# Optimization experiments

Measured on AMD Instinct MI355X. Metric: run time of the kernel, lower is better.

## Reference

```python
import jax, jax.numpy as jnp
import numpy as np

DIM_Q, DIM_K, HEADS = 256, 32, 4
SCALE = (DIM_Q // HEADS) ** (-0.5)


def setup_inputs() -> dict:
    key = jax.random.key(0)
    ks = jax.random.split(key, 12)
    B, C, H, W, D = 2, DIM_Q, 16, 16, 16
    inp = {
        'F_VNet': jax.random.normal(ks[0], (B, C, H, W, D), dtype=jnp.float32),
        'F_Knowledge': jax.random.normal(ks[1], (B, DIM_K, H, W, D), dtype=jnp.float32),
        # torch nn.Linear: y = x @ W.T + b, W: [out, in]
        'Wq': jax.random.normal(ks[2], (DIM_Q, DIM_Q), dtype=jnp.float32) * (DIM_Q ** -0.5),
        'bq': jnp.zeros((DIM_Q,), dtype=jnp.float32),
        'Wk': jax.random.normal(ks[3], (DIM_Q, DIM_K), dtype=jnp.float32) * (DIM_K ** -0.5),
        'bk': jnp.zeros((DIM_Q,), dtype=jnp.float32),
        'Wv': jax.random.normal(ks[4], (DIM_Q, DIM_K), dtype=jnp.float32) * (DIM_K ** -0.5),
        'bv': jnp.zeros((DIM_Q,), dtype=jnp.float32),
        'Wo': jax.random.normal(ks[5], (DIM_Q, DIM_Q), dtype=jnp.float32) * (DIM_Q ** -0.5),
        'bo': jnp.zeros((DIM_Q,), dtype=jnp.float32),
    }
    return inp


def reference(F_VNet, F_Knowledge, Wq, bq, Wk, bk, Wv, bv, Wo, bo):
    B, C, H, W, D = F_VNet.shape
    Ck = F_Knowledge.shape[1]
    # flatten spatial dims to tokens: [B, N, C]
    xq = F_VNet.reshape(B, C, -1).transpose(0, 2, 1)          # [B, Nq, dim_q]
    xk = F_Knowledge.reshape(B, Ck, -1).transpose(0, 2, 1)    # [B, Nk, dim_k]
    Q = xq @ Wq.T + bq                                        # [B, Nq, dim_q]
    K = xk @ Wk.T + bk                                        # [B, Nk, dim_q]
    V = xk @ Wv.T + bv                                        # [B, Nk, dim_q]
    attn = jax.nn.softmax(jnp.einsum('bqc,bkc->bqk', Q, K) * SCALE, axis=-1)
    out = jnp.einsum('bqk,bkc->bqc', attn, V)                 # [B, Nq, dim_q]
    out = out @ Wo.T + bo
    out = out.transpose(0, 2, 1).reshape(B, C, H, W, D)
    return F_VNet + out
```

## Files before the change

kernel.cpp:

```cpp
#include <hip/hip_runtime.h>
#include <hip/hip_bf16.h>
#include <cstdint>
#include <cstddef>

#define N_TOK 4096
#define CQ    256
#define CK    32

typedef __attribute__((ext_vector_type(4))) float  f32x4;
typedef __attribute__((ext_vector_type(8))) __bf16 bf16x8;
typedef __attribute__((ext_vector_type(4))) short  s16x4;

__device__ __forceinline__ unsigned short f2bf(float f) {
  union { float f; unsigned u; } x; x.f = f;
  unsigned r = x.u + 0x7FFFu + ((x.u >> 16) & 1u);
  return (unsigned short)(r >> 16);
}

__device__ __forceinline__ f32x4 mfma16(bf16x8 a, bf16x8 b, f32x4 c) {
  return __builtin_amdgcn_mfma_f32_16x16x32_bf16(a, b, c, 0, 0, 0);
}

__device__ __forceinline__ int pos2key(int pos) {
  return ((pos >> 3) << 2) + (pos & 3) + (((pos >> 2) & 1) << 4);
}

__global__ __launch_bounds__(256) void prep_kernel(
    const float* __restrict__ Wq, const float* __restrict__ bq,
    const float* __restrict__ Wk, const float* __restrict__ Wv,
    const float* __restrict__ bv, const float* __restrict__ Wo,
    const float* __restrict__ bo, const float* __restrict__ Fk,
    unsigned short* __restrict__ Aqkt, float* __restrict__ bqk,
    unsigned short* __restrict__ W2bf, float* __restrict__ c2,
    unsigned short* __restrict__ Vpv, unsigned short* __restrict__ XkT)
{
  __shared__ float red[256];
  __shared__ unsigned short trs[128][33];
  const int blk = blockIdx.x, t = threadIdx.x;
  if (blk < 32) {
    const int j = blk;
    float acc = 0.f;
    #pragma unroll 8
    for (int i = 0; i < CQ; i++)
      acc = fmaf(Wq[(size_t)i * CQ + t], Wk[(size_t)i * CK + j], acc);
    Aqkt[(size_t)j * CQ + t] = f2bf(0.125f * acc);
    red[t] = bq[t] * Wk[(size_t)t * CK + j];
    __syncthreads();
    for (int s = 128; s > 0; s >>= 1) {
      if (t < s) red[t] += red[t + s];
      __syncthreads();
    }
    if (t == 0) bqk[j] = 0.125f * red[0];
  } else if (blk < 64) {
    const int j = blk - 32;
    float acc = 0.f, acc2 = 0.f;
    #pragma unroll 8
    for (int i = 0; i < CQ; i++) {
      float wo = Wo[(size_t)t * CQ + i];
      acc  = fmaf(wo, Wv[(size_t)i * CK + j], acc);
      acc2 = fmaf(wo, bv[i], acc2);
    }
    W2bf[(size_t)t * CK + j] = f2bf(acc);
    if (j == 0) c2[t] = bo[t] + acc2;
  } else {
    const int blk2 = blk - 64;
    const int b = blk2 >> 5;
    const int t0 = (blk2 & 31) << 7;
    #pragma unroll
    for (int i = 0; i < 4; i++) {
      int flat = (i * 256 + t) << 2;
      int r = flat >> 7, c4 = flat & 127;
      float4 v = *(const float4*)(Fk + ((size_t)(b * CK + r)) * N_TOK + t0 + c4);
      ushort4 u = { f2bf(v.x), f2bf(v.y), f2bf(v.z), f2bf(v.w) };
      trs[c4][r] = u.x; trs[c4+1][r] = u.y; trs[c4+2][r] = u.z; trs[c4+3][r] = u.w;
    }
    __syncthreads();
    {
      const int token = t >> 1, half = t & 1;
      unsigned short tmp[16] __attribute__((aligned(16)));
      #pragma unroll
      for (int k = 0; k < 16; k++) tmp[k] = trs[token][half * 16 + k];
      unsigned short* dst = XkT + ((size_t)(b * N_TOK + t0 + token)) * CK + half * 16;
      ((uint4*)dst)[0] = ((const uint4*)tmp)[0];
      ((uint4*)dst)[1] = ((const uint4*)tmp)[1];
    }
    {
      const int ch32l = t >> 6, d = (t & 63) >> 1, ph = t & 1;
      unsigned short tmp[16] __attribute__((aligned(16)));
      #pragma unroll
      for (int i = 0; i < 16; i++) {
        int pos = ph * 16 + i;
        tmp[i] = trs[ch32l * 32 + pos2key(pos)][d];
      }
      unsigned short* dst = Vpv +
          (((size_t)(b * 128 + (t0 >> 5) + ch32l)) * 32 + d) * 32 + ph * 16;
      ((uint4*)dst)[0] = ((const uint4*)tmp)[0];
      ((uint4*)dst)[1] = ((const uint4*)tmp)[1];
    }
  }
}

__global__ __launch_bounds__(128) void qproj_kernel(
    const float* __restrict__ X, const unsigned short* __restrict__ Aqkt,
    const float* __restrict__ bqk, unsigned short* __restrict__ QN)
{
  __shared__ unsigned short bs[32][40];
  const int b = blockIdx.x >> 7;
  const int t0 = (blockIdx.x & 127) << 5;
  const int t = threadIdx.x, w = t >> 6;
  const int lane = t & 63, c = lane & 15, g = lane >> 4;
  f32x4 acc[2] = {};
  for (int k0 = 0; k0 < CQ; k0 += 32) {
    #pragma unroll
    for (int i = 0; i < 2; i++) {
      int flat = (i * 128 + t) << 2;
      int cc = flat >> 5, tk = flat & 31;
      float4 v = *(const float4*)(X + ((size_t)(b * CQ + k0 + cc)) * N_TOK + t0 + tk);
      bs[tk  ][cc] = f2bf(v.x); bs[tk+1][cc] = f2bf(v.y);
      bs[tk+2][cc] = f2bf(v.z); bs[tk+3][cc] = f2bf(v.w);
    }
    __syncthreads();
    bf16x8 a = *(const bf16x8*)&bs[w * 16 + c][g * 8];
    #pragma unroll
    for (int nt = 0; nt < 2; nt++) {
      bf16x8 bB = *(const bf16x8*)(Aqkt + (size_t)(nt * 16 + c) * CQ + k0 + g * 8);
      acc[nt] = mfma16(a, bB, acc[nt]);
    }
    __syncthreads();
  }
  #pragma unroll
  for (int nt = 0; nt < 2; nt++) {
    float bj = bqk[nt * 16 + c];
    #pragma unroll
    for (int r = 0; r < 4; r++)
      QN[((size_t)(b * N_TOK + t0 + w * 16 + g * 4 + r)) * CK + nt * 16 + c] =
          f2bf(acc[nt][r] + bj);
  }
}

__global__ __launch_bounds__(256, 4) void flash_kernel(
    const unsigned short* __restrict__ QN, const unsigned short* __restrict__ XkT,
    const unsigned short* __restrict__ Vpv, float* __restrict__ partO,
    float* __restrict__ partML)
{
  __shared__ unsigned short ks[512 * 40] __attribute__((aligned(16)));
  const int blk = blockIdx.x;
  const int b   = blk >> 9;
  const int qg  = (blk >> 3) & 63;
  const int ksp = blk & 7;
  const int t = threadIdx.x, w = t >> 6;
  const int lane = t & 63, c = lane & 15, g = lane >> 4;
  const int t0 = qg * 64 + w * 16;
  const int gk0 = ksp * 512;

  {
    const unsigned short* src = XkT + ((size_t)(b * N_TOK + gk0)) * CK;
    #pragma unroll
    for (int r = 0; r < 8; r++) {
      int flat = r * 256 + t;
      int row = flat >> 2, part = flat & 3;
      *(uint4*)(ks + row * 40 + part * 8) = *(const uint4*)(src + (size_t)flat * 8);
    }
  }
  const bf16x8 qf = *(const bf16x8*)(QN + ((size_t)(b * N_TOK + t0 + c)) * CK + g * 8);
  __syncthreads();

  const unsigned short* vp = Vpv + (size_t)b * 128 * 1024;
  float mO = -1e30f, lO = 0.f;
  f32x4 O0 = {}, O1 = {};

  #pragma unroll
  for (int pass = 0; pass < 2; pass++) {
    const int pk = pass * 256;

    f32x4 s[4][4];
    #pragma unroll
    for (int it = 0; it < 4; it++)
      #pragma unroll
      for (int nt = 0; nt < 4; nt++) {
        bf16x8 ak = *(const bf16x8*)&ks[(pk + it * 64 + nt * 16 + c) * 40 + g * 8];
        f32x4 z = {};
        s[it][nt] = mfma16(ak, qf, z);
      }

    float mx = -1e30f;
    #pragma unroll
    for (int it = 0; it < 4; it++)
      #pragma unroll
      for (int nt = 0; nt < 4; nt++)
        mx = fmaxf(mx, fmaxf(fmaxf(s[it][nt][0], s[it][nt][1]),
                             fmaxf(s[it][nt][2], s[it][nt][3])));
    mx = fmaxf(mx, __shfl_xor(mx, 16));
    mx = fmaxf(mx, __shfl_xor(mx, 32));

    float l = 0.f;
    s16x4 pf[4][4];
    #pragma unroll
    for (int it = 0; it < 4; it++)
      #pragma unroll
      for (int nt = 0; nt < 4; nt++) {
        float p0 = __expf(s[it][nt][0] - mx);
        float p1 = __expf(s[it][nt][1] - mx);
        float p2 = __expf(s[it][nt][2] - mx);
        float p3 = __expf(s[it][nt][3] - mx);
        l += (p0 + p1) + (p2 + p3);
        union { __hip_bfloat162 h2[2]; s16x4 v; } pu;
        pu.h2[0] = __float22bfloat162_rn(make_float2(p0, p1));
        pu.h2[1] = __float22bfloat162_rn(make_float2(p2, p3));
        pf[it][nt] = pu.v;
      }
    l += __shfl_xor(l, 16);
    l += __shfl_xor(l, 32);

    f32x4 o0 = {}, o1 = {};
    #pragma unroll
    for (int it = 0; it < 4; it++)
      #pragma unroll
      for (int ntp = 0; ntp < 2; ntp++) {
        const int ch32 = (gk0 + pk + it * 64 + ntp * 32) >> 5;
        const unsigned short* base = vp + (size_t)ch32 * 1024;
        union { s16x4 h[2]; bf16x8 v; } bu;
        bu.h[0] = pf[it][ntp * 2];
        bu.h[1] = pf[it][ntp * 2 + 1];
        bf16x8 a0 = *(const bf16x8*)(base + c * 32 + g * 8);
        bf16x8 a1 = *(const bf16x8*)(base + (16 + c) * 32 + g * 8);
        o0 = mfma16(a0, bu.v, o0);
        o1 = mfma16(a1, bu.v, o1);
      }

    float mN = fmaxf(mO, mx);
    float fO = __expf(mO - mN), fP = __expf(mx - mN);
    lO = lO * fO + l * fP;
    #pragma unroll
    for (int r = 0; r < 4; r++) {
      O0[r] = O0[r] * fO + o0[r] * fP;
      O1[r] = O1[r] * fO + o1[r] * fP;
    }
    mO = mN;
  }

  float* po = partO + (size_t)blk * 2048 + (w * 16 + c) * 32;
  *(f32x4*)(po + g * 4)      = O0;
  *(f32x4*)(po + 16 + g * 4) = O1;
  if (lane < 16) {
    partML[(size_t)blk * 128 + w * 16 + lane]      = mO;
    partML[(size_t)blk * 128 + 64 + w * 16 + lane] = lO;
  }
}

__global__ __launch_bounds__(256) void oproj_kernel(
    const float* __restrict__ partO, const float* __restrict__ partML,
    const unsigned short* __restrict__ W2bf, const float* __restrict__ c2,
    const float* __restrict__ X, float* __restrict__ Y)
{
  __shared__ unsigned short ons[32][40];
  const int blk = blockIdx.x;
  const int b = blk >> 7, tt = blk & 127;
  const int t = threadIdx.x, w = t >> 6;
  const int lane = t & 63, c = lane & 15, g = lane >> 4;
  const int t0 = tt * 32;

  {
    const int tl32 = t >> 3, ch4 = t & 7;
    const int q  = t0 + tl32;
    const int qg = q >> 6, tl = q & 63;
    const int blkbase = (b << 9) + qg * 8;
    float mv[8], lv[8], mM = -1e30f;
    #pragma unroll
    for (int k = 0; k < 8; k++) {
      mv[k] = partML[(size_t)(blkbase + k) * 128 + tl];
      lv[k] = partML[(size_t)(blkbase + k) * 128 + 64 + tl];
      mM = fmaxf(mM, mv[k]);
    }
    float lsum = 0.f, f[8];
    #pragma unroll
    for (int k = 0; k < 8; k++) {
      f[k] = __expf(mv[k] - mM);
      lsum = fmaf(f[k], lv[k], lsum);
    }
    const float inv = 1.0f / lsum;
    float acc[4] = {};
    #pragma unroll
    for (int k = 0; k < 8; k++) {
      float4 v = *(const float4*)(partO + (size_t)(blkbase + k) * 2048 + tl * 32 + ch4 * 4);
      acc[0] = fmaf(f[k], v.x, acc[0]); acc[1] = fmaf(f[k], v.y, acc[1]);
      acc[2] = fmaf(f[k], v.z, acc[2]); acc[3] = fmaf(f[k], v.w, acc[3]);
    }
    ons[tl32][ch4 * 4    ] = f2bf(acc[0] * inv);
    ons[tl32][ch4 * 4 + 1] = f2bf(acc[1] * inv);
    ons[tl32][ch4 * 4 + 2] = f2bf(acc[2] * inv);
    ons[tl32][ch4 * 4 + 3] = f2bf(acc[3] * inv);
  }
  __syncthreads();

  const int m0 = w * 64;
  bf16x8 bB[2];
  #pragma unroll
  for (int nt = 0; nt < 2; nt++)
    bB[nt] = *(const bf16x8*)&ons[nt * 16 + c][g * 8];
  f32x4 acc[4][2] = {};
  #pragma unroll
  for (int mt = 0; mt < 4; mt++) {
    bf16x8 aW = *(const bf16x8*)(W2bf + (size_t)(m0 + mt * 16 + c) * CK + g * 8);
    acc[mt][0] = mfma16(aW, bB[0], acc[mt][0]);
    acc[mt][1] = mfma16(aW, bB[1], acc[mt][1]);
  }
  #pragma unroll
  for (int mt = 0; mt < 4; mt++)
    #pragma unroll
    for (int r = 0; r < 4; r++) {
      const int row = m0 + mt * 16 + g * 4 + r;
      const float cc = c2[row];
      #pragma unroll
      for (int nt = 0; nt < 2; nt++) {
        size_t idx = ((size_t)(b * CQ + row)) * N_TOK + t0 + nt * 16 + c;
        Y[idx] = acc[mt][nt][r] + cc + X[idx];
      }
    }
}

extern "C" void kernel_launch(void* const* d_in, const int* in_sizes, int n_in,
                              void* d_out, int out_size, void* d_ws, size_t ws_size,
                              hipStream_t stream) {
  const float* F  = (const float*)d_in[0];
  const float* Fk = (const float*)d_in[1];
  const float* Wq = (const float*)d_in[2];
  const float* bq = (const float*)d_in[3];
  const float* Wk = (const float*)d_in[4];
  const float* Wv = (const float*)d_in[6];
  const float* bv = (const float*)d_in[7];
  const float* Wo = (const float*)d_in[8];
  const float* bo = (const float*)d_in[9];
  float* Y = (float*)d_out;
  char* ws = (char*)d_ws;
  unsigned short* XkT   = (unsigned short*)(ws);
  unsigned short* Vpv   = (unsigned short*)(ws + (512u << 10));
  unsigned short* QN    = (unsigned short*)(ws + (1536u << 10));
  unsigned short* Aqkt  = (unsigned short*)(ws + (2048u << 10));
  unsigned short* W2bf  = (unsigned short*)(ws + (2080u << 10));
  float*          bqk   = (float*)(ws + (2112u << 10));
  float*          c2    = (float*)(ws + (2116u << 10));
  float*          partO = (float*)(ws + (4096u << 10));
  float*          partML= (float*)(ws + (16384u << 10));

  prep_kernel <<<128,  256, 0, stream>>>(Wq, bq, Wk, Wv, bv, Wo, bo, Fk,
                                         Aqkt, bqk, W2bf, c2, Vpv, XkT);
  qproj_kernel<<<256,  128, 0, stream>>>(F, Aqkt, bqk, QN);
  flash_kernel<<<1024, 256, 0, stream>>>(QN, XkT, Vpv, partO, partML);
  oproj_kernel<<<256,  256, 0, stream>>>(partO, partML, W2bf, c2, F, Y);
}
```

Baseline: 129.4 us.

## Fuse Q projection, flash attention and output projection into one kernel

Merges the qproj, flash-attention and oproj kernels into a single fused kernel. Each 32-query block computes Q in LDS, streams all 4096 keys in 8 chunks with register double-buffering, splits the key range across two wave pairs, merges their partial softmax states in LDS, then applies the output projection and residual. This removes the partO/partML round trips, the QN buffer and two launches. The trade-off is a grid of only 256 blocks at one block per CU, which lowers parallelism compared with the 1024-block split-K flash kernel. The softmax scale now folds log2(e) so exp2 can be used, and two prep unroll factors change.

```diff
diff --git a/kernel.cpp b/kernel.cpp
--- a/kernel.cpp
+++ b/kernel.cpp
@@ -6,6 +6,7 @@
 #define N_TOK 4096
 #define CQ    256
 #define CK    32
+#define QK_SCALE 0.18033688011112042f
 
 typedef __attribute__((ext_vector_type(4))) float  f32x4;
 typedef __attribute__((ext_vector_type(8))) __bf16 bf16x8;
@@ -19,6 +20,19 @@
 
 __device__ __forceinline__ f32x4 mfma16(bf16x8 a, bf16x8 b, f32x4 c) {
   return __builtin_amdgcn_mfma_f32_16x16x32_bf16(a, b, c, 0, 0, 0);
+}
+
+__device__ __forceinline__ float exp2fast(float x) {
+#if __has_builtin(__builtin_amdgcn_exp2f)
+  return __builtin_amdgcn_exp2f(x);
+#else
+  float r; asm("v_exp_f32 %0, %1" : "=v"(r) : "v"(x)); return r;
+#endif
+}
+
+__device__ __forceinline__ void bar_lds() {
+  asm volatile("s_waitcnt lgkmcnt(0)" ::: "memory");
+  __builtin_amdgcn_s_barrier();
 }
 
 __device__ __forceinline__ int pos2key(int pos) {
@@ -40,21 +54,21 @@
   if (blk < 32) {
     const int j = blk;
     float acc = 0.f;
-    #pragma unroll 8
+    #pragma unroll 16
     for (int i = 0; i < CQ; i++)
       acc = fmaf(Wq[(size_t)i * CQ + t], Wk[(size_t)i * CK + j], acc);
-    Aqkt[(size_t)j * CQ + t] = f2bf(0.125f * acc);
+    Aqkt[(size_t)j * CQ + t] = f2bf(QK_SCALE * acc);
     red[t] = bq[t] * Wk[(size_t)t * CK + j];
     __syncthreads();
     for (int s = 128; s > 0; s >>= 1) {
       if (t < s) red[t] += red[t + s];
       __syncthreads();
     }
-    if (t == 0) bqk[j] = 0.125f * red[0];
+    if (t == 0) bqk[j] = QK_SCALE * red[0];
   } else if (blk < 64) {
     const int j = blk - 32;
     float acc = 0.f, acc2 = 0.f;
-    #pragma unroll 8
+    #pragma unroll 16
     for (int i = 0; i < CQ; i++) {
       float wo = Wo[(size_t)t * CQ + i];
       acc  = fmaf(wo, Wv[(size_t)i * CK + j], acc);
@@ -100,87 +114,95 @@
   }
 }
 
-__global__ __launch_bounds__(128) void qproj_kernel(
+__global__ __launch_bounds__(256, 1) void fused_kernel(
     const float* __restrict__ X, const unsigned short* __restrict__ Aqkt,
-    const float* __restrict__ bqk, unsigned short* __restrict__ QN)
+    const float* __restrict__ bqk, const unsigned short* __restrict__ XkT,
+    const unsigned short* __restrict__ Vpv,
+    const unsigned short* __restrict__ W2bf, const float* __restrict__ c2,
+    float* __restrict__ Y)
 {
-  __shared__ unsigned short bs[32][40];
-  const int b = blockIdx.x >> 7;
+  __shared__ union {
+    unsigned short ks[512 * 40];
+    unsigned short bs8[8][32][40];
+  } u __attribute__((aligned(16)));
+  __shared__ unsigned short qn[32][40] __attribute__((aligned(16)));
+  __shared__ float mlx[2][2][16];
+  __shared__ float ofx[2][16][32];
+
+  const int b  = blockIdx.x >> 7;
   const int t0 = (blockIdx.x & 127) << 5;
   const int t = threadIdx.x, w = t >> 6;
   const int lane = t & 63, c = lane & 15, g = lane >> 4;
-  f32x4 acc[2] = {};
-  for (int k0 = 0; k0 < CQ; k0 += 32) {
-    #pragma unroll
-    for (int i = 0; i < 2; i++) {
-      int flat = (i * 128 + t) << 2;
-      int cc = flat >> 5, tk = flat & 31;
-      float4 v = *(const float4*)(X + ((size_t)(b * CQ + k0 + cc)) * N_TOK + t0 + tk);
-      bs[tk  ][cc] = f2bf(v.x); bs[tk+1][cc] = f2bf(v.y);
-      bs[tk+2][cc] = f2bf(v.z); bs[tk+3][cc] = f2bf(v.w);
-    }
-    __syncthreads();
-    bf16x8 a = *(const bf16x8*)&bs[w * 16 + c][g * 8];
+  const int tw = w & 1, kh = w >> 1;
+  const int pk = kh << 8;
+
+  #pragma unroll
+  for (int i = 0; i < 8; i++) {
+    int flat = i * 256 + t;
+    int cc = flat >> 3, tk = (flat & 7) << 2;
+    float4 v = *(const float4*)(X + ((size_t)(b * CQ + cc)) * N_TOK + t0 + tk);
+    int kk = cc >> 5, chl = cc & 31;
+    u.bs8[kk][tk    ][chl] = f2bf(v.x);
+    u.bs8[kk][tk + 1][chl] = f2bf(v.y);
+    u.bs8[kk][tk + 2][chl] = f2bf(v.z);
+    u.bs8[kk][tk + 3][chl] = f2bf(v.w);
+  }
+  const unsigned short* xksrc = XkT + ((size_t)b * N_TOK) * CK;
+  uint4 R[8];
+  #pragma unroll
+  for (int r = 0; r < 8; r++)
+    R[r] = *(const uint4*)(xksrc + (size_t)(r * 256 + t) * 8);
+  bar_lds();
+
+  if (w < 2) {
+    f32x4 qacc[2] = {};
+    #pragma unroll
+    for (int kk = 0; kk < 8; kk++) {
+      bf16x8 a = *(const bf16x8*)&u.bs8[kk][w * 16 + c][g * 8];
+      #pragma unroll
+      for (int nt = 0; nt < 2; nt++) {
+        bf16x8 bB = *(const bf16x8*)(Aqkt + (size_t)(nt * 16 + c) * CQ + kk * 32 + g * 8);
+        qacc[nt] = mfma16(a, bB, qacc[nt]);
+      }
+    }
     #pragma unroll
     for (int nt = 0; nt < 2; nt++) {
-      bf16x8 bB = *(const bf16x8*)(Aqkt + (size_t)(nt * 16 + c) * CQ + k0 + g * 8);
-      acc[nt] = mfma16(a, bB, acc[nt]);
-    }
-    __syncthreads();
-  }
-  #pragma unroll
-  for (int nt = 0; nt < 2; nt++) {
-    float bj = bqk[nt * 16 + c];
-    #pragma unroll
-    for (int r = 0; r < 4; r++)
-      QN[((size_t)(b * N_TOK + t0 + w * 16 + g * 4 + r)) * CK + nt * 16 + c] =
-          f2bf(acc[nt][r] + bj);
-  }
-}
-
-__global__ __launch_bounds__(256, 4) void flash_kernel(
-    const unsigned short* __restrict__ QN, const unsigned short* __restrict__ XkT,
-    const unsigned short* __restrict__ Vpv, float* __restrict__ partO,
-    float* __restrict__ partML)
-{
-  __shared__ unsigned short ks[512 * 40] __attribute__((aligned(16)));
-  const int blk = blockIdx.x;
-  const int b   = blk >> 9;
-  const int qg  = (blk >> 3) & 63;
-  const int ksp = blk & 7;
-  const int t = threadIdx.x, w = t >> 6;
-  const int lane = t & 63, c = lane & 15, g = lane >> 4;
-  const int t0 = qg * 64 + w * 16;
-  const int gk0 = ksp * 512;
-
-  {
-    const unsigned short* src = XkT + ((size_t)(b * N_TOK + gk0)) * CK;
+      float bj = bqk[nt * 16 + c];
+      #pragma unroll
+      for (int r = 0; r < 4; r++)
+        qn[w * 16 + g * 4 + r][nt * 16 + c] = f2bf(qacc[nt][r] + bj);
+    }
+  }
+  bar_lds();
+
+  const bf16x8 qf = *(const bf16x8*)&qn[tw * 16 + c][g * 8];
+  const unsigned short* vp = Vpv + (size_t)b * 128 * 1024;
+
+  float mO = -1e30f, lO = 0.f;
+  f32x4 O0 = {}, O1 = {};
+
+  for (int s = 0; s < 8; s++) {
     #pragma unroll
     for (int r = 0; r < 8; r++) {
       int flat = r * 256 + t;
-      int row = flat >> 2, part = flat & 3;
-      *(uint4*)(ks + row * 40 + part * 8) = *(const uint4*)(src + (size_t)flat * 8);
-    }
-  }
-  const bf16x8 qf = *(const bf16x8*)(QN + ((size_t)(b * N_TOK + t0 + c)) * CK + g * 8);
-  __syncthreads();
-
-  const unsigned short* vp = Vpv + (size_t)b * 128 * 1024;
-  float mO = -1e30f, lO = 0.f;
-  f32x4 O0 = {}, O1 = {};
-
-  #pragma unroll
-  for (int pass = 0; pass < 2; pass++) {
-    const int pk = pass * 256;
-
-    f32x4 s[4][4];
+      *(uint4*)(u.ks + (flat >> 2) * 40 + (flat & 3) * 8) = R[r];
+    }
+    if (s < 7) {
+      const unsigned short* nsrc = xksrc + (size_t)(s + 1) * (512 * CK);
+      #pragma unroll
+      for (int r = 0; r < 8; r++)
+        R[r] = *(const uint4*)(nsrc + (size_t)(r * 256 + t) * 8);
+    }
+    bar_lds();
+
+    f32x4 sc[4][4];
     #pragma unroll
     for (int it = 0; it < 4; it++)
       #pragma unroll
       for (int nt = 0; nt < 4; nt++) {
-        bf16x8 ak = *(const bf16x8*)&ks[(pk + it * 64 + nt * 16 + c) * 40 + g * 8];
+        bf16x8 ak = *(const bf16x8*)&u.ks[(pk + it * 64 + nt * 16 + c) * 40 + g * 8];
         f32x4 z = {};
-        s[it][nt] = mfma16(ak, qf, z);
+        sc[it][nt] = mfma16(ak, qf, z);
       }
 
     float mx = -1e30f;
@@ -188,8 +210,8 @@
     for (int it = 0; it < 4; it++)
       #pragma unroll
       for (int nt = 0; nt < 4; nt++)
-        mx = fmaxf(mx, fmaxf(fmaxf(s[it][nt][0], s[it][nt][1]),
-                             fmaxf(s[it][nt][2], s[it][nt][3])));
+        mx = fmaxf(mx, fmaxf(fmaxf(sc[it][nt][0], sc[it][nt][1]),
+                             fmaxf(sc[it][nt][2], sc[it][nt][3])));
     mx = fmaxf(mx, __shfl_xor(mx, 16));
     mx = fmaxf(mx, __shfl_xor(mx, 32));
 
@@ -199,10 +221,10 @@
     for (int it = 0; it < 4; it++)
       #pragma unroll
       for (int nt = 0; nt < 4; nt++) {
-        float p0 = __expf(s[it][nt][0] - mx);
-        float p1 = __expf(s[it][nt][1] - mx);
-        float p2 = __expf(s[it][nt][2] - mx);
-        float p3 = __expf(s[it][nt][3] - mx);
+        float p0 = exp2fast(sc[it][nt][0] - mx);
+        float p1 = exp2fast(sc[it][nt][1] - mx);
+        float p2 = exp2fast(sc[it][nt][2] - mx);
+        float p3 = exp2fast(sc[it][nt][3] - mx);
         l += (p0 + p1) + (p2 + p3);
         union { __hip_bfloat162 h2[2]; s16x4 v; } pu;
         pu.h2[0] = __float22bfloat162_rn(make_float2(p0, p1));
@@ -217,7 +239,7 @@
     for (int it = 0; it < 4; it++)
       #pragma unroll
       for (int ntp = 0; ntp < 2; ntp++) {
-        const int ch32 = (gk0 + pk + it * 64 + ntp * 32) >> 5;
+        const int ch32 = (s << 4) + (kh << 3) + it * 2 + ntp;
         const unsigned short* base = vp + (size_t)ch32 * 1024;
         union { s16x4 h[2]; bf16x8 v; } bu;
         bu.h[0] = pf[it][ntp * 2];
@@ -229,7 +251,7 @@
       }
 
     float mN = fmaxf(mO, mx);
-    float fO = __expf(mO - mN), fP = __expf(mx - mN);
+    float fO = exp2fast(mO - mN), fP = exp2fast(mx - mN);
     lO = lO * fO + l * fP;
     #pragma unroll
     for (int r = 0; r < 4; r++) {
@@ -237,84 +259,54 @@
       O1[r] = O1[r] * fO + o1[r] * fP;
     }
     mO = mN;
-  }
-
-  float* po = partO + (size_t)blk * 2048 + (w * 16 + c) * 32;
-  *(f32x4*)(po + g * 4)      = O0;
-  *(f32x4*)(po + 16 + g * 4) = O1;
-  if (lane < 16) {
-    partML[(size_t)blk * 128 + w * 16 + lane]      = mO;
-    partML[(size_t)blk * 128 + 64 + w * 16 + lane] = lO;
-  }
-}
-
-__global__ __launch_bounds__(256) void oproj_kernel(
-    const float* __restrict__ partO, const float* __restrict__ partML,
-    const unsigned short* __restrict__ W2bf, const float* __restrict__ c2,
-    const float* __restrict__ X, float* __restrict__ Y)
-{
-  __shared__ unsigned short ons[32][40];
-  const int blk = blockIdx.x;
-  const int b = blk >> 7, tt = blk & 127;
-  const int t = threadIdx.x, w = t >> 6;
-  const int lane = t & 63, c = lane & 15, g = lane >> 4;
-  const int t0 = tt * 32;
-
-  {
-    const int tl32 = t >> 3, ch4 = t & 7;
-    const int q  = t0 + tl32;
-    const int qg = q >> 6, tl = q & 63;
-    const int blkbase = (b << 9) + qg * 8;
-    float mv[8], lv[8], mM = -1e30f;
-    #pragma unroll
-    for (int k = 0; k < 8; k++) {
-      mv[k] = partML[(size_t)(blkbase + k) * 128 + tl];
-      lv[k] = partML[(size_t)(blkbase + k) * 128 + 64 + tl];
-      mM = fmaxf(mM, mv[k]);
-    }
-    float lsum = 0.f, f[8];
-    #pragma unroll
-    for (int k = 0; k < 8; k++) {
-      f[k] = __expf(mv[k] - mM);
-      lsum = fmaf(f[k], lv[k], lsum);
-    }
-    const float inv = 1.0f / lsum;
-    float acc[4] = {};
-    #pragma unroll
-    for (int k = 0; k < 8; k++) {
-      float4 v = *(const float4*)(partO + (size_t)(blkbase + k) * 2048 + tl * 32 + ch4 * 4);
-      acc[0] = fmaf(f[k], v.x, acc[0]); acc[1] = fmaf(f[k], v.y, acc[1]);
-      acc[2] = fmaf(f[k], v.z, acc[2]); acc[3] = fmaf(f[k], v.w, acc[3]);
-    }
-    ons[tl32][ch4 * 4    ] = f2bf(acc[0] * inv);
-    ons[tl32][ch4 * 4 + 1] = f2bf(acc[1] * inv);
-    ons[tl32][ch4 * 4 + 2] = f2bf(acc[2] * inv);
-    ons[tl32][ch4 * 4 + 3] = f2bf(acc[3] * inv);
+    bar_lds();
+  }
+
+  if (kh == 1) {
+    if (lane < 16) { mlx[tw][0][c] = mO; mlx[tw][1][c] = lO; }
+    #pragma unroll
+    for (int r = 0; r < 4; r++) {
+      ofx[tw][c][g * 4 + r]      = O0[r];
+      ofx[tw][c][16 + g * 4 + r] = O1[r];
+    }
   }
   __syncthreads();
+  if (kh == 0) {
+    float m1 = mlx[tw][0][c], l1 = mlx[tw][1][c];
+    float mN = fmaxf(mO, m1);
+    float f0 = exp2fast(mO - mN), f1 = exp2fast(m1 - mN);
+    float inv = 1.0f / (lO * f0 + l1 * f1);
+    f0 *= inv; f1 *= inv;
+    #pragma unroll
+    for (int r = 0; r < 4; r++) {
+      qn[tw * 16 + c][g * 4 + r]      = f2bf(O0[r] * f0 + ofx[tw][c][g * 4 + r] * f1);
+      qn[tw * 16 + c][16 + g * 4 + r] = f2bf(O1[r] * f0 + ofx[tw][c][16 + g * 4 + r] * f1);
+    }
+  }
+  __syncthreads();
 
   const int m0 = w * 64;
-  bf16x8 bB[2];
+  bf16x8 wb[2];
   #pragma unroll
   for (int nt = 0; nt < 2; nt++)
-    bB[nt] = *(const bf16x8*)&ons[nt * 16 + c][g * 8];
-  f32x4 acc[4][2] = {};
+    wb[nt] = *(const bf16x8*)&qn[nt * 16 + c][g * 8];
+  f32x4 acc2[4][2] = {};
   #pragma unroll
   for (int mt = 0; mt < 4; mt++) {
     bf16x8 aW = *(const bf16x8*)(W2bf + (size_t)(m0 + mt * 16 + c) * CK + g * 8);
-    acc[mt][0] = mfma16(aW, bB[0], acc[mt][0]);
-    acc[mt][1] = mfma16(aW, bB[1], acc[mt][1]);
+    acc2[mt][0] = mfma16(aW, wb[0], acc2[mt][0]);
+    acc2[mt][1] = mfma16(aW, wb[1], acc2[mt][1]);
   }
   #pragma unroll
   for (int mt = 0; mt < 4; mt++)
     #pragma unroll
     for (int r = 0; r < 4; r++) {
       const int row = m0 + mt * 16 + g * 4 + r;
-      const float cc = c2[row];
+      const float cc2 = c2[row];
       #pragma unroll
       for (int nt = 0; nt < 2; nt++) {
         size_t idx = ((size_t)(b * CQ + row)) * N_TOK + t0 + nt * 16 + c;
-        Y[idx] = acc[mt][nt][r] + cc + X[idx];
+        Y[idx] = acc2[mt][nt][r] + cc2 + X[idx];
       }
     }
 }
@@ -335,17 +327,12 @@
   char* ws = (char*)d_ws;
   unsigned short* XkT   = (unsigned short*)(ws);
   unsigned short* Vpv   = (unsigned short*)(ws + (512u << 10));
-  unsigned short* QN    = (unsigned short*)(ws + (1536u << 10));
   unsigned short* Aqkt  = (unsigned short*)(ws + (2048u << 10));
   unsigned short* W2bf  = (unsigned short*)(ws + (2080u << 10));
   float*          bqk   = (float*)(ws + (2112u << 10));
   float*          c2    = (float*)(ws + (2116u << 10));
-  float*          partO = (float*)(ws + (4096u << 10));
-  float*          partML= (float*)(ws + (16384u << 10));
-
-  prep_kernel <<<128,  256, 0, stream>>>(Wq, bq, Wk, Wv, bv, Wo, bo, Fk,
-                                         Aqkt, bqk, W2bf, c2, Vpv, XkT);
-  qproj_kernel<<<256,  128, 0, stream>>>(F, Aqkt, bqk, QN);
-  flash_kernel<<<1024, 256, 0, stream>>>(QN, XkT, Vpv, partO, partML);
-  oproj_kernel<<<256,  256, 0, stream>>>(partO, partML, W2bf, c2, F, Y);
-}
+
+  prep_kernel <<<128, 256, 0, stream>>>(Wq, bq, Wk, Wv, bv, Wo, bo, Fk,
+                                        Aqkt, bqk, W2bf, c2, Vpv, XkT);
+  fused_kernel<<<256, 256, 0, stream>>>(F, Aqkt, bqk, XkT, Vpv, W2bf, c2, Y);
+}
```

New measurement: 120.6 us. -6.8%, faster.
